# Performance work log

Hardware: AMD Instinct MI355X
Metric: run time of the kernel (lower is better)

Reference implementation:

```python
import jax, jax.numpy as jnp
import numpy as np

N = 50000      # nodes
E = 800000     # edges (before self loops)
F_IN = 64
H = 128
OUT = 1
G = 512        # graphs in batch
NEG_SLOPE = 0.2


def setup_inputs() -> dict:
    key = jax.random.key(0)
    ks = jax.random.split(key, 16)
    s_in = 1.0 / np.sqrt(F_IN)
    s_h = 1.0 / np.sqrt(H)
    return {
        "x": jax.random.normal(ks[0], (N, F_IN), jnp.float32),
        "edge_index": jax.random.randint(ks[1], (2, E), 0, N, jnp.int64),
        "edge_weight": jax.random.uniform(ks[2], (E,), jnp.float32),
        "batch": jnp.sort(jax.random.randint(ks[3], (N,), 0, G, jnp.int64)),
        # GATv2 layer 1 (lin_l, lin_r, att, bias)
        "Wl1": jax.random.normal(ks[4], (F_IN, H), jnp.float32) * s_in,
        "bl1": jnp.zeros((H,), jnp.float32),
        "Wr1": jax.random.normal(ks[5], (F_IN, H), jnp.float32) * s_in,
        "br1": jnp.zeros((H,), jnp.float32),
        "att1": jax.random.normal(ks[6], (H,), jnp.float32) * s_h,
        "b1": jnp.zeros((H,), jnp.float32),
        # GATv2 layer 2
        "Wl2": jax.random.normal(ks[7], (H, H), jnp.float32) * s_h,
        "bl2": jnp.zeros((H,), jnp.float32),
        "Wr2": jax.random.normal(ks[8], (H, H), jnp.float32) * s_h,
        "br2": jnp.zeros((H,), jnp.float32),
        "att2": jax.random.normal(ks[9], (H,), jnp.float32) * s_h,
        "b2": jnp.zeros((H,), jnp.float32),
        # final linear head
        "Wlin": jax.random.normal(ks[10], (H, OUT), jnp.float32) * s_h,
        "blin": jnp.zeros((OUT,), jnp.float32),
    }


def gatv2_conv(x, src, dst, Wl, bl, Wr, br, att, bias):
    """PyG GATv2Conv, heads=1: alpha = softmax_dst(att . leaky_relu(xl[src]+xr[dst]));
    out[dst] = sum alpha * xl[src] + bias. Self loops already in (src, dst)."""
    xl = x @ Wl + bl                       # [N,H]  source transform
    xr = x @ Wr + br                       # [N,H]  destination transform
    e = xl[src] + xr[dst]                  # [Etot,H]
    logits = jax.nn.leaky_relu(e, NEG_SLOPE) @ att   # [Etot]
    # segment softmax over destination nodes (self loops -> every node nonempty)
    m = jax.ops.segment_max(logits, dst, num_segments=N)
    ea = jnp.exp(logits - m[dst])
    denom = jax.ops.segment_sum(ea, dst, num_segments=N)
    alpha = ea / denom[dst]
    out = jax.ops.segment_sum(alpha[:, None] * xl[src], dst, num_segments=N)
    return out + bias


def reference(x, edge_index, edge_weight, batch,
              Wl1, bl1, Wr1, br1, att1, b1,
              Wl2, bl2, Wr2, br2, att2, b2,
              Wlin, blin):
    # add self loops (GATv2Conv default add_self_loops=True); edge_weight unused by GATv2
    loops = jnp.arange(N, dtype=edge_index.dtype)
    src = jnp.concatenate([edge_index[0], loops])
    dst = jnp.concatenate([edge_index[1], loops])

    h = jax.nn.relu(gatv2_conv(x, src, dst, Wl1, bl1, Wr1, br1, att1, b1))
    h = jax.nn.relu(gatv2_conv(h, src, dst, Wl2, bl2, Wr2, br2, att2, b2))

    # global mean pool over graphs
    sums = jax.ops.segment_sum(h, batch, num_segments=G)          # [G,H]
    cnt = jax.ops.segment_sum(jnp.ones((N,), h.dtype), batch, num_segments=G)
    pooled = sums / jnp.maximum(cnt, 1.0)[:, None]

    return pooled @ Wlin + blin                                   # [G,OUT]
```

## Files before the change

### kernel.cpp

```cpp
#include <hip/hip_runtime.h>
#include <hip/hip_fp16.h>
#include <math.h>

#define N_NODES 50000
#define N_EDGES 800000
#define F_IN    64
#define H_DIM   128
#define N_GRAPH 512
#define NEG_SLOPE 0.2f
#define SCAN_NB ((N_NODES + 255) / 256)

typedef __attribute__((ext_vector_type(8))) short short8;
typedef __attribute__((ext_vector_type(4))) float f32x4;
typedef __attribute__((ext_vector_type(2))) float f32x2;

__device__ __forceinline__ void bsplit(float v, unsigned short& h, unsigned short& l) {
    unsigned u = __float_as_uint(v);
    h = (unsigned short)(u >> 16);
    float hf = __uint_as_float(u & 0xFFFF0000u);
    float r = v - hf;
    l = (unsigned short)(__float_as_uint(r) >> 16);
}
__device__ __forceinline__ float bjoin(unsigned short h, unsigned short l) {
    return __uint_as_float(((unsigned)h) << 16) + __uint_as_float(((unsigned)l) << 16);
}

#define NB_PX 3125
#define NB_PW 192
#define NB_H  3125
__global__ __launch_bounds__(256) void k_prep(
    const float* __restrict__ x,
    const float* __restrict__ Wl1, const float* __restrict__ Wr1,
    const float* __restrict__ Wl2, const float* __restrict__ Wr2,
    const int* __restrict__ dst,
    unsigned short* __restrict__ Xhi, unsigned short* __restrict__ Xlo,
    unsigned short* __restrict__ WThi, unsigned short* __restrict__ WTlo,
    int* __restrict__ counts, int* __restrict__ rank)
{
    const int bid = blockIdx.x, tid = threadIdx.x;
    if (bid < NB_PX) {
        int i4 = (bid * 256 + tid) * 4;
        if (i4 < N_NODES * F_IN) {
            float4 v = *(const float4*)(x + i4);
            ushort4 h, l;
            bsplit(v.x, h.x, l.x); bsplit(v.y, h.y, l.y);
            bsplit(v.z, h.z, l.z); bsplit(v.w, h.w, l.w);
            *(ushort4*)(Xhi + i4) = h;
            *(ushort4*)(Xlo + i4) = l;
        }
    } else if (bid < NB_PX + NB_PW) {
        int idx = (bid - NB_PX) * 256 + tid;
        if (idx < 49152) {
            const float* W; int K, li, base, o;
            if (idx < 8192)       { W = Wl1; K = 64;  li = idx;         base = 0;     o = 0; }
            else if (idx < 16384) { W = Wr1; K = 64;  li = idx - 8192;  base = 0;     o = 1; }
            else if (idx < 32768) { W = Wl2; K = 128; li = idx - 16384; base = 16384; o = 0; }
            else                  { W = Wr2; K = 128; li = idx - 32768; base = 16384; o = 1; }
            int c = li / K, k = li - c * K;
            int g = c >> 4, n16 = c & 15;
            int kkblk = k >> 5, quad = (k >> 3) & 3, j = k & 7;
            int off = base + kkblk * 8192 + o * 4096 + g * 512 + (quad * 16 + n16) * 8 + j;
            unsigned short h, l;
            bsplit(W[k * 128 + c], h, l);
            WThi[off] = h; WTlo[off] = l;
        }
    } else {
        int e = (bid - NB_PX - NB_PW) * 256 + tid;
        if (e < N_EDGES) {
            int pos = atomicAdd(&counts[dst[e]], 1);
            rank[e] = pos;
        }
    }
}

__global__ __launch_bounds__(256) void k_scan1(const int* __restrict__ counts,
                                               int* __restrict__ excl,
                                               int* __restrict__ partials) {
    __shared__ int s[256];
    int t = threadIdx.x, gid = blockIdx.x * 256 + t;
    int v = (gid < N_NODES) ? counts[gid] : 0;
    s[t] = v;
    __syncthreads();
    for (int off = 1; off < 256; off <<= 1) {
        int x = (t >= off) ? s[t - off] : 0;
        __syncthreads();
        s[t] += x;
        __syncthreads();
    }
    if (gid < N_NODES) excl[gid] = s[t] - v;
    if (t == 255) partials[blockIdx.x] = s[t];
}

__global__ __launch_bounds__(256) void k_scan3(int* __restrict__ offsets,
                                               const int* __restrict__ partials) {
    __shared__ int s[256];
    const int t = threadIdx.x, b = blockIdx.x;
    int v = (t < SCAN_NB) ? partials[t] : 0;
    s[t] = v;
    __syncthreads();
    for (int off = 1; off < 256; off <<= 1) {
        int x = (t >= off) ? s[t - off] : 0;
        __syncthreads();
        s[t] += x;
        __syncthreads();
    }
    int base = (b > 0) ? s[b - 1] : 0;
    int gid = b * 256 + t;
    if (gid < N_NODES) offsets[gid] += base;
    if (gid == 0) offsets[N_NODES] = N_EDGES;
}

__global__ __launch_bounds__(256) void k_fill(const int* __restrict__ src,
                                              const int* __restrict__ dst,
                                              const int* __restrict__ offsets,
                                              const int* __restrict__ rank,
                                              int* __restrict__ col_src) {
    int e = blockIdx.x * 256 + threadIdx.x;
    if (e < N_EDGES) {
        col_src[offsets[dst[e]] + rank[e]] = src[e];
    }
}

#define APITCH 40
#define GB_GEMM ((N_NODES + 63) / 64)
__global__ __launch_bounds__(256, 4) void k_gemm_mfma(
    const unsigned short* __restrict__ Xhi, const unsigned short* __restrict__ Xlo,
    const unsigned short* __restrict__ WThi, const unsigned short* __restrict__ WTlo,
    const float* __restrict__ bl, const float* __restrict__ br,
    unsigned short* __restrict__ OL, unsigned short* __restrict__ OR_, int K)
{
    __shared__ __align__(16) unsigned short Ah[64 * APITCH];
    __shared__ __align__(16) unsigned short Al[64 * APITCH];

    const int tid  = threadIdx.x;
    const int wv   = tid >> 6;
    const int lane = tid & 63;
    const int n16  = lane & 15;
    const int quad = lane >> 4;
    const int row0 = blockIdx.x * 64;

    f32x4 acc[4][2][2];
#pragma unroll
    for (int r = 0; r < 4; ++r)
#pragma unroll
        for (int c = 0; c < 2; ++c)
#pragma unroll
            for (int o = 0; o < 2; ++o) acc[r][c][o] = (f32x4)0.f;

    for (int kk = 0; kk < K; kk += 32) {
#pragma unroll
        for (int jj = 0; jj < 2; ++jj) {
            int j = tid + jj * 256;
            int part = j >> 8;
            int r = (j & 255) >> 2, sub = j & 3;
            int grow = row0 + r;
            const unsigned short* s = (part ? Xlo : Xhi) + (size_t)grow * K + kk + sub * 8;
            unsigned short* dl = (part ? Al : Ah) + r * APITCH + sub * 8;
            uint4 v = make_uint4(0u, 0u, 0u, 0u);
            if (grow < N_NODES) v = *(const uint4*)s;
            *(uint4*)dl = v;
        }
        __syncthreads();

        const unsigned short* wb_h = WThi + (size_t)(kk >> 5) * 8192;
        const unsigned short* wb_l = WTlo + (size_t)(kk >> 5) * 8192;
        short8 bh[2][2], bo[2][2];
#pragma unroll
        for (int c = 0; c < 2; ++c)
#pragma unroll
            for (int o = 0; o < 2; ++o) {
                size_t off = (size_t)o * 4096 + (size_t)(wv * 2 + c) * 512 + (size_t)lane * 8;
                bh[c][o] = *(const short8*)(wb_h + off);
                bo[c][o] = *(const short8*)(wb_l + off);
            }
#pragma unroll
        for (int r = 0; r < 4; ++r) {
            int rl = r * 16 + n16;
            short8 ah = *(const short8*)(Ah + rl * APITCH + quad * 8);
            short8 al = *(const short8*)(Al + rl * APITCH + quad * 8);
#pragma unroll
            for (int c = 0; c < 2; ++c)
#pragma unroll
                for (int o = 0; o < 2; ++o) {
                    f32x4 t = acc[r][c][o];
                    t = __builtin_amdgcn_mfma_f32_16x16x32_bf16(ah, bh[c][o], t, 0, 0, 0);
                    t = __builtin_amdgcn_mfma_f32_16x16x32_bf16(ah, bo[c][o], t, 0, 0, 0);
                    t = __builtin_amdgcn_mfma_f32_16x16x32_bf16(al, bh[c][o], t, 0, 0, 0);
                    acc[r][c][o] = t;
                }
        }
        __syncthreads();
    }

#pragma unroll
    for (int r = 0; r < 4; ++r)
#pragma unroll
        for (int c = 0; c < 2; ++c)
#pragma unroll
            for (int o = 0; o < 2; ++o) {
                int col = wv * 32 + c * 16 + n16;
                float bb = (o ? br : bl)[col];
                unsigned short* O = o ? OR_ : OL;
#pragma unroll
                for (int g = 0; g < 4; ++g) {
                    int grow = row0 + r * 16 + quad * 4 + g;
                    if (grow < N_NODES) {
                        __half hv = __float2half(acc[r][c][o][g] + bb);
                        O[(size_t)grow * 128 + col] = *(unsigned short*)&hv;
                    }
                }
            }
}

__device__ __forceinline__ float red16dpp(float v) {
    v += __int_as_float(__builtin_amdgcn_update_dpp(
             0, __float_as_int(v), 0xB1, 0xF, 0xF, true));
    v += __int_as_float(__builtin_amdgcn_update_dpp(
             0, __float_as_int(v), 0x4E, 0xF, 0xF, true));
    v += __int_as_float(__builtin_amdgcn_update_dpp(
             0, __float_as_int(v), 0x141, 0xF, 0xF, true));
    v += __int_as_float(__builtin_amdgcn_update_dpp(
             0, __float_as_int(v), 0x140, 0xF, 0xF, true));
    return v;
}

__device__ __forceinline__ void load_h8v(const unsigned short* base, size_t off,
                                         f32x2 x[4]) {
    uint4 u = *(const uint4*)(base + off);
    float2 a = __half22float2(*(__half2*)&u.x);
    float2 b = __half22float2(*(__half2*)&u.y);
    float2 c = __half22float2(*(__half2*)&u.z);
    float2 d = __half22float2(*(__half2*)&u.w);
    f32x2 v0 = {a.x, a.y}; x[0] = v0;
    f32x2 v1 = {b.x, b.y}; x[1] = v1;
    f32x2 v2 = {c.x, c.y}; x[2] = v2;
    f32x2 v3 = {d.x, d.y}; x[3] = v3;
}

__device__ __forceinline__ float dot8lk(const f32x2 x[4], const f32x2 r[4],
                                        const f32x2 a[4]) {
    f32x2 e0 = x[0] + r[0];
    f32x2 e1 = x[1] + r[1];
    f32x2 l0 = __builtin_elementwise_max(e0, NEG_SLOPE * e0);
    f32x2 l1 = __builtin_elementwise_max(e1, NEG_SLOPE * e1);
    f32x2 s0 = a[0] * l0;
    f32x2 s1 = a[1] * l1;
    f32x2 e2 = x[2] + r[2];
    f32x2 e3 = x[3] + r[3];
    f32x2 l2 = __builtin_elementwise_max(e2, NEG_SLOPE * e2);
    f32x2 l3 = __builtin_elementwise_max(e3, NEG_SLOPE * e3);
    s0 += a[2] * l2;
    s1 += a[3] * l3;
    f32x2 s = s0 + s1;
    return s.x + s.y;
}

__global__ __launch_bounds__(256) void k_edge(
    const unsigned short* __restrict__ xl, const unsigned short* __restrict__ xr,
    const float* __restrict__ att, const float* __restrict__ bias,
    const int* __restrict__ offsets, const int* __restrict__ col_src,
    unsigned short* __restrict__ outHi, unsigned short* __restrict__ outLo)
{
    int d = blockIdx.x * 4 + (threadIdx.x >> 6);
    if (d >= N_NODES) return;
    const int lane = threadIdx.x & 63;
    const int q = lane >> 4;
    const int t = lane & 15;
    const size_t dim0 = (size_t)t * 8;

    f32x2 rr[4], aa[4], xs[4];
    load_h8v(xr, (size_t)d * 128 + dim0, rr);
    {
        const float4 a0 = *(const float4*)(att + dim0);
        const float4 a1 = *(const float4*)(att + dim0 + 4);
        f32x2 w0 = {a0.x, a0.y}; aa[0] = w0;
        f32x2 w1 = {a0.z, a0.w}; aa[1] = w1;
        f32x2 w2 = {a1.x, a1.y}; aa[2] = w2;
        f32x2 w3 = {a1.z, a1.w}; aa[3] = w3;
    }
    load_h8v(xl, (size_t)d * 128 + dim0, xs);
    float sl = red16dpp(dot8lk(xs, rr, aa));

    float m = sl, thr = sl + 8.f;
    float lsum = (q == 0) ? 1.f : 0.f;
    f32x2 zero = {0.f, 0.f};
    f32x2 acc[4];
#pragma unroll
    for (int j = 0; j < 4; ++j) acc[j] = (q == 0) ? xs[j] : zero;

    const int ibeg = offsets[d], iend = offsets[d + 1];
    for (int base = ibeg; base < iend; base += 4) {
        int i = base + q;
        bool valid = (i < iend);
        int s = valid ? col_src[i] : d;
        f32x2 x[4];
        load_h8v(xl, (size_t)s * 128 + dim0, x);
        float logit = red16dpp(dot8lk(x, rr, aa));
        if (__builtin_expect(logit > thr, 0)) {
            float sc = __expf(m - logit);
            lsum *= sc;
#pragma unroll
            for (int j = 0; j < 4; ++j) acc[j] = acc[j] * sc;
            m = logit; thr = logit + 8.f;
        }
        float w = valid ? __expf(logit - m) : 0.f;
        lsum += w;
        f32x2 w2 = {w, w};
#pragma unroll
        for (int j = 0; j < 4; ++j) acc[j] += w2 * x[j];
    }

    float M = m;
    M = fmaxf(M, __shfl_xor(M, 16));
    M = fmaxf(M, __shfl_xor(M, 32));
    float sc = __expf(m - M);
    lsum *= sc;
    f32x2 sc2 = {sc, sc};
#pragma unroll
    for (int j = 0; j < 4; ++j) acc[j] = acc[j] * sc2;
#pragma unroll
    for (int off = 16; off <= 32; off <<= 1) {
        lsum += __shfl_xor(lsum, off);
#pragma unroll
        for (int j = 0; j < 4; ++j) {
            acc[j].x += __shfl_xor(acc[j].x, off);
            acc[j].y += __shfl_xor(acc[j].y, off);
        }
    }

    if (q == 0) {
        float inv = 1.f / lsum;
        const float4 b0 = *(const float4*)(bias + dim0);
        const float4 b1 = *(const float4*)(bias + dim0 + 4);
        float bv[8] = {b0.x, b0.y, b0.z, b0.w, b1.x, b1.y, b1.z, b1.w};
        float v[8];
#pragma unroll
        for (int j = 0; j < 4; ++j) {
            v[2 * j]     = fmaxf(fmaf(acc[j].x, inv, bv[2 * j]), 0.f);
            v[2 * j + 1] = fmaxf(fmaf(acc[j].y, inv, bv[2 * j + 1]), 0.f);
        }
        union { unsigned short s[8]; uint4 u; } Hh, Ll;
#pragma unroll
        for (int i2 = 0; i2 < 8; ++i2) bsplit(v[i2], Hh.s[i2], Ll.s[i2]);
        *(uint4*)(outHi + (size_t)d * 128 + dim0) = Hh.u;
        *(uint4*)(outLo + (size_t)d * 128 + dim0) = Ll.u;
    }
}

__global__ __launch_bounds__(256) void k_pool(
    const unsigned short* __restrict__ hHi, const unsigned short* __restrict__ hLo,
    const int* __restrict__ batch,
    float* __restrict__ psum, float* __restrict__ pcnt)
{
    const int tid = threadIdx.x;
    const int tx = tid & 31;
    const int ty = tid >> 5;
    const int n0 = blockIdx.x * 64;
    const int d0 = tx * 4;

    float4 acc = make_float4(0.f, 0.f, 0.f, 0.f);
    int cur = -1, crun = 0;
#pragma unroll
    for (int it = 0; it < 8; ++it) {
        int n = n0 + it * 8 + ty;
        if (n < N_NODES) {
            int g = batch[n];
            if (g != cur) {
                if (cur >= 0) {
                    atomicAdd(&psum[cur * 128 + d0 + 0], acc.x);
                    atomicAdd(&psum[cur * 128 + d0 + 1], acc.y);
                    atomicAdd(&psum[cur * 128 + d0 + 2], acc.z);
                    atomicAdd(&psum[cur * 128 + d0 + 3], acc.w);
                    if (tx == 0) atomicAdd(&pcnt[cur], (float)crun);
                }
                cur = g; acc = make_float4(0.f, 0.f, 0.f, 0.f); crun = 0;
            }
            ushort4 h = *(const ushort4*)(hHi + (size_t)n * 128 + d0);
            ushort4 l = *(const ushort4*)(hLo + (size_t)n * 128 + d0);
            acc.x += bjoin(h.x, l.x);
            acc.y += bjoin(h.y, l.y);
            acc.z += bjoin(h.z, l.z);
            acc.w += bjoin(h.w, l.w);
            crun++;
        }
    }
    if (cur >= 0) {
        atomicAdd(&psum[cur * 128 + d0 + 0], acc.x);
        atomicAdd(&psum[cur * 128 + d0 + 1], acc.y);
        atomicAdd(&psum[cur * 128 + d0 + 2], acc.z);
        atomicAdd(&psum[cur * 128 + d0 + 3], acc.w);
        if (tx == 0) atomicAdd(&pcnt[cur], (float)crun);
    }
}

__global__ __launch_bounds__(256) void k_head(
    const float* __restrict__ psum, const float* __restrict__ pcnt,
    const float* __restrict__ Wlin, const float* __restrict__ blin,
    float* __restrict__ out)
{
    int g = blockIdx.x * 4 + (threadIdx.x >> 6);
    if (g >= N_GRAPH) return;
    int lane = threadIdx.x & 63;
    float c = fmaxf(pcnt[g], 1.f);
    float2 s = *(const float2*)(psum + (size_t)g * 128 + lane * 2);
    float p = (s.x * Wlin[lane * 2] + s.y * Wlin[lane * 2 + 1]) / c;
#pragma unroll
    for (int off = 32; off > 0; off >>= 1) p += __shfl_xor(p, off);
    if (lane == 0) out[g] = p + blin[0];
}

extern "C" void kernel_launch(void* const* d_in, const int* in_sizes, int n_in,
                              void* d_out, int out_size, void* d_ws, size_t ws_size,
                              hipStream_t stream) {
    const float* x     = (const float*)d_in[0];
    const int*   ei    = (const int*)d_in[1];
    const int*   batch = (const int*)d_in[3];
    const float* Wl1 = (const float*)d_in[4],  *bl1 = (const float*)d_in[5];
    const float* Wr1 = (const float*)d_in[6],  *br1 = (const float*)d_in[7];
    const float* att1= (const float*)d_in[8],  *b1  = (const float*)d_in[9];
    const float* Wl2 = (const float*)d_in[10], *bl2 = (const float*)d_in[11];
    const float* Wr2 = (const float*)d_in[12], *br2 = (const float*)d_in[13];
    const float* att2= (const float*)d_in[14], *b2  = (const float*)d_in[15];
    const float* Wlin= (const float*)d_in[16], *blin= (const float*)d_in[17];
    float* out = (float*)d_out;

    const int* src = ei;
    const int* dst = ei + N_EDGES;

    char* p = (char*)d_ws;
    auto carve = [&](size_t bytes) {
        void* r = (void*)p;
        p += (bytes + 255) & ~(size_t)255;
        return r;
    };
    unsigned short* bufA   = (unsigned short*)carve((size_t)N_NODES * 128 * 2);
    unsigned short* bufB   = (unsigned short*)carve((size_t)N_NODES * 128 * 2);
    unsigned short* Hhi    = (unsigned short*)carve((size_t)N_NODES * 128 * 2);
    unsigned short* Hlo    = (unsigned short*)carve((size_t)N_NODES * 128 * 2);
    unsigned short* Xhi1   = (unsigned short*)carve((size_t)N_NODES * 64 * 2);
    unsigned short* Xlo1   = (unsigned short*)carve((size_t)N_NODES * 64 * 2);
    unsigned short* WThi   = (unsigned short*)carve(49152 * 2);
    unsigned short* WTlo   = (unsigned short*)carve(49152 * 2);
    int*            offsets= (int*)carve((size_t)(N_NODES + 1) * 4);
    int*            rank   = (int*)carve((size_t)N_EDGES * 4);
    int*            partials=(int*)carve(256 * 4);
    int*            col_src= (int*)carve((size_t)N_EDGES * 4);
    char* zb = (char*)carve(200192 + 262144 + 2048);
    int*   counts = (int*)zb;
    float* psum   = (float*)(zb + 200192);
    float* pcnt   = (float*)(zb + 200192 + 262144);
    const size_t zbytes = 200192 + 262144 + 2048;

    hipMemsetAsync(zb, 0, zbytes, stream);

    k_prep<<<NB_PX + NB_PW + NB_H, 256, 0, stream>>>(
        x, Wl1, Wr1, Wl2, Wr2, dst,
        Xhi1, Xlo1, WThi, WTlo, counts, rank);
    k_scan1<<<SCAN_NB, 256, 0, stream>>>(counts, offsets, partials);
    k_scan3<<<SCAN_NB, 256, 0, stream>>>(offsets, partials);
    k_fill <<<(N_EDGES + 255) / 256, 256, 0, stream>>>(src, dst, offsets, rank, col_src);

    k_gemm_mfma<<<GB_GEMM, 256, 0, stream>>>(Xhi1, Xlo1, WThi, WTlo,
                                             bl1, br1, bufA, bufB, F_IN);
    k_edge<<<(N_NODES + 3) / 4, 256, 0, stream>>>(
        bufA, bufB, att1, b1, offsets, col_src, Hhi, Hlo);
    k_gemm_mfma<<<GB_GEMM, 256, 0, stream>>>(Hhi, Hlo, WThi + 16384, WTlo + 16384,
                                             bl2, br2, bufA, bufB, H_DIM);
    k_edge<<<(N_NODES + 3) / 4, 256, 0, stream>>>(
        bufA, bufB, att2, b2, offsets, col_src, Hhi, Hlo);
    k_pool<<<(N_NODES + 63) / 64, 256, 0, stream>>>(Hhi, Hlo, batch, psum, pcnt);
    k_head<<<(N_GRAPH + 3) / 4, 256, 0, stream>>>(psum, pcnt, Wlin, blin, out);
}
```

Before: 304.3 us.

## Fuse dst histogram into first GEMM launch and pad counters to cache lines

Moves the per-edge atomic histogram out of the prep kernel and into extra blocks of the first-layer GEMM launch, so the atomic-heavy edge counting can run alongside the MFMA GEMM blocks. The per-node counters are also spaced 16 ints apart (one 64-byte slot each) to reduce atomic contention and false sharing on shared cache lines. The cost is a larger memset (3.2MB instead of 200KB) and strided reads in the scan.

```diff
diff --git a/kernel.cpp b/kernel.cpp
--- a/kernel.cpp
+++ b/kernel.cpp
@@ -27,15 +27,12 @@
 
 #define NB_PX 3125
 #define NB_PW 192
-#define NB_H  3125
 __global__ __launch_bounds__(256) void k_prep(
     const float* __restrict__ x,
     const float* __restrict__ Wl1, const float* __restrict__ Wr1,
     const float* __restrict__ Wl2, const float* __restrict__ Wr2,
-    const int* __restrict__ dst,
     unsigned short* __restrict__ Xhi, unsigned short* __restrict__ Xlo,
-    unsigned short* __restrict__ WThi, unsigned short* __restrict__ WTlo,
-    int* __restrict__ counts, int* __restrict__ rank)
+    unsigned short* __restrict__ WThi, unsigned short* __restrict__ WTlo)
 {
     const int bid = blockIdx.x, tid = threadIdx.x;
     if (bid < NB_PX) {
@@ -48,7 +45,7 @@
             *(ushort4*)(Xhi + i4) = h;
             *(ushort4*)(Xlo + i4) = l;
         }
-    } else if (bid < NB_PX + NB_PW) {
+    } else {
         int idx = (bid - NB_PX) * 256 + tid;
         if (idx < 49152) {
             const float* W; int K, li, base, o;
@@ -64,12 +61,6 @@
             bsplit(W[k * 128 + c], h, l);
             WThi[off] = h; WTlo[off] = l;
         }
-    } else {
-        int e = (bid - NB_PX - NB_PW) * 256 + tid;
-        if (e < N_EDGES) {
-            int pos = atomicAdd(&counts[dst[e]], 1);
-            rank[e] = pos;
-        }
     }
 }
 
@@ -78,7 +69,7 @@
                                                int* __restrict__ partials) {
     __shared__ int s[256];
     int t = threadIdx.x, gid = blockIdx.x * 256 + t;
-    int v = (gid < N_NODES) ? counts[gid] : 0;
+    int v = (gid < N_NODES) ? counts[gid << 4] : 0;
     s[t] = v;
     __syncthreads();
     for (int off = 1; off < 256; off <<= 1) {
@@ -123,21 +114,22 @@
 
 #define APITCH 40
 #define GB_GEMM ((N_NODES + 63) / 64)
-__global__ __launch_bounds__(256, 4) void k_gemm_mfma(
+#define GB_HIST ((N_EDGES + 255) / 256)
+
+__device__ __forceinline__ void gemm_body(
+    unsigned short* __restrict__ Ah, unsigned short* __restrict__ Al,
     const unsigned short* __restrict__ Xhi, const unsigned short* __restrict__ Xlo,
     const unsigned short* __restrict__ WThi, const unsigned short* __restrict__ WTlo,
     const float* __restrict__ bl, const float* __restrict__ br,
-    unsigned short* __restrict__ OL, unsigned short* __restrict__ OR_, int K)
-{
-    __shared__ __align__(16) unsigned short Ah[64 * APITCH];
-    __shared__ __align__(16) unsigned short Al[64 * APITCH];
-
+    unsigned short* __restrict__ OL, unsigned short* __restrict__ OR_,
+    int K, int blk)
+{
     const int tid  = threadIdx.x;
     const int wv   = tid >> 6;
     const int lane = tid & 63;
     const int n16  = lane & 15;
     const int quad = lane >> 4;
-    const int row0 = blockIdx.x * 64;
+    const int row0 = blk * 64;
 
     f32x4 acc[4][2][2];
 #pragma unroll
@@ -210,6 +202,36 @@
                     }
                 }
             }
+}
+
+__global__ __launch_bounds__(256, 4) void k_gemm_mfma(
+    const unsigned short* __restrict__ Xhi, const unsigned short* __restrict__ Xlo,
+    const unsigned short* __restrict__ WThi, const unsigned short* __restrict__ WTlo,
+    const float* __restrict__ bl, const float* __restrict__ br,
+    unsigned short* __restrict__ OL, unsigned short* __restrict__ OR_, int K)
+{
+    __shared__ __align__(16) unsigned short Ah[64 * APITCH];
+    __shared__ __align__(16) unsigned short Al[64 * APITCH];
+    gemm_body(Ah, Al, Xhi, Xlo, WThi, WTlo, bl, br, OL, OR_, K, blockIdx.x);
+}
+
+__global__ __launch_bounds__(256, 4) void k_gemm1_hist(
+    const unsigned short* __restrict__ Xhi, const unsigned short* __restrict__ Xlo,
+    const unsigned short* __restrict__ WThi, const unsigned short* __restrict__ WTlo,
+    const float* __restrict__ bl, const float* __restrict__ br,
+    unsigned short* __restrict__ OL, unsigned short* __restrict__ OR_, int K,
+    const int* __restrict__ dst, int* __restrict__ counts, int* __restrict__ rank)
+{
+    __shared__ __align__(16) unsigned short Ah[64 * APITCH];
+    __shared__ __align__(16) unsigned short Al[64 * APITCH];
+    if (blockIdx.x < GB_GEMM) {
+        gemm_body(Ah, Al, Xhi, Xlo, WThi, WTlo, bl, br, OL, OR_, K, blockIdx.x);
+    } else {
+        int e = (blockIdx.x - GB_GEMM) * 256 + threadIdx.x;
+        if (e < N_EDGES) {
+            rank[e] = atomicAdd(&counts[dst[e] << 4], 1);
+        }
+    }
 }
 
 __device__ __forceinline__ float red16dpp(float v) {
@@ -445,23 +467,26 @@
     int*            rank   = (int*)carve((size_t)N_EDGES * 4);
     int*            partials=(int*)carve(256 * 4);
     int*            col_src= (int*)carve((size_t)N_EDGES * 4);
-    char* zb = (char*)carve(200192 + 262144 + 2048);
+    const size_t counts_bytes = (size_t)N_NODES * 64;
+    char* zb = (char*)carve(counts_bytes + 262144 + 2048);
     int*   counts = (int*)zb;
-    float* psum   = (float*)(zb + 200192);
-    float* pcnt   = (float*)(zb + 200192 + 262144);
-    const size_t zbytes = 200192 + 262144 + 2048;
+    float* psum   = (float*)(zb + counts_bytes);
+    float* pcnt   = (float*)(zb + counts_bytes + 262144);
+    const size_t zbytes = counts_bytes + 262144 + 2048;
 
     hipMemsetAsync(zb, 0, zbytes, stream);
 
-    k_prep<<<NB_PX + NB_PW + NB_H, 256, 0, stream>>>(
-        x, Wl1, Wr1, Wl2, Wr2, dst,
-        Xhi1, Xlo1, WThi, WTlo, counts, rank);
+    k_prep<<<NB_PX + NB_PW, 256, 0, stream>>>(
+        x, Wl1, Wr1, Wl2, Wr2, Xhi1, Xlo1, WThi, WTlo);
+
+    k_gemm1_hist<<<GB_GEMM + GB_HIST, 256, 0, stream>>>(
+        Xhi1, Xlo1, WThi, WTlo, bl1, br1, bufA, bufB, F_IN,
+        dst, counts, rank);
+
     k_scan1<<<SCAN_NB, 256, 0, stream>>>(counts, offsets, partials);
     k_scan3<<<SCAN_NB, 256, 0, stream>>>(offsets, partials);
     k_fill <<<(N_EDGES + 255) / 256, 256, 0, stream>>>(src, dst, offsets, rank, col_src);
 
-    k_gemm_mfma<<<GB_GEMM, 256, 0, stream>>>(Xhi1, Xlo1, WThi, WTlo,
-                                             bl1, br1, bufA, bufB, F_IN);
     k_edge<<<(N_NODES + 3) / 4, 256, 0, stream>>>(
         bufA, bufB, att1, b1, offsets, col_src, Hhi, Hlo);
     k_gemm_mfma<<<GB_GEMM, 256, 0, stream>>>(Hhi, Hlo, WThi + 16384, WTlo + 16384,
```

Result: no change. 299.5 us (-1.6%).

## Build CSR with two-level LDS bin sort instead of global atomic counting

Applied to the files above, without the earlier changes.

Replaces the per-destination global atomicAdd counting sort with a two-level bucket sort. Edges are first binned into 256-node buckets using shared-memory atomics per 2048-edge block. A block-major scan then gives bucket offsets, and a per-bucket kernel sorts edges locally by destination and writes CSR offsets and source indices. Source and local destination are packed into one 32-bit word, which relies on node ids fitting in 16 bits. The first GEMM is also launched before the CSR build so it no longer waits on it. The final stage runs only 196 blocks, which may underuse the GPU, and it adds more kernel launches.

```diff
diff --git a/kernel.cpp b/kernel.cpp
--- a/kernel.cpp
+++ b/kernel.cpp
@@ -8,11 +8,15 @@
 #define H_DIM   128
 #define N_GRAPH 512
 #define NEG_SLOPE 0.2f
-#define SCAN_NB ((N_NODES + 255) / 256)
 
 typedef __attribute__((ext_vector_type(8))) short short8;
 typedef __attribute__((ext_vector_type(4))) float f32x4;
 typedef __attribute__((ext_vector_type(2))) float f32x2;
+
+#define NBIN   196
+#define NBLK1  391
+#define NBB    (NBIN * NBLK1)
+#define SCANA_NB ((NBB + 255) / 256)
 
 __device__ __forceinline__ void bsplit(float v, unsigned short& h, unsigned short& l) {
     unsigned u = __float_as_uint(v);
@@ -27,7 +31,6 @@
 
 #define NB_PX 3125
 #define NB_PW 192
-#define NB_H  3125
 __global__ __launch_bounds__(256) void k_prep(
     const float* __restrict__ x,
     const float* __restrict__ Wl1, const float* __restrict__ Wr1,
@@ -35,8 +38,9 @@
     const int* __restrict__ dst,
     unsigned short* __restrict__ Xhi, unsigned short* __restrict__ Xlo,
     unsigned short* __restrict__ WThi, unsigned short* __restrict__ WTlo,
-    int* __restrict__ counts, int* __restrict__ rank)
+    int* __restrict__ lrank, int* __restrict__ bcnt)
 {
+    __shared__ int cnt_lds[NBIN];
     const int bid = blockIdx.x, tid = threadIdx.x;
     if (bid < NB_PX) {
         int i4 = (bid * 256 + tid) * 4;
@@ -65,20 +69,28 @@
             WThi[off] = h; WTlo[off] = l;
         }
     } else {
-        int e = (bid - NB_PX - NB_PW) * 256 + tid;
-        if (e < N_EDGES) {
-            int pos = atomicAdd(&counts[dst[e]], 1);
-            rank[e] = pos;
-        }
-    }
-}
-
-__global__ __launch_bounds__(256) void k_scan1(const int* __restrict__ counts,
-                                               int* __restrict__ excl,
+        const int b2 = bid - NB_PX - NB_PW;
+        if (tid < NBIN) cnt_lds[tid] = 0;
+        __syncthreads();
+#pragma unroll
+        for (int it = 0; it < 8; ++it) {
+            int e = b2 * 2048 + it * 256 + tid;
+            if (e < N_EDGES) {
+                int d = dst[e];
+                lrank[e] = atomicAdd(&cnt_lds[d >> 8], 1);
+            }
+        }
+        __syncthreads();
+        if (tid < NBIN) bcnt[tid * NBLK1 + b2] = cnt_lds[tid];
+    }
+}
+
+__global__ __launch_bounds__(256) void k_scanA(const int* __restrict__ bcnt,
+                                               int* __restrict__ bbase,
                                                int* __restrict__ partials) {
     __shared__ int s[256];
     int t = threadIdx.x, gid = blockIdx.x * 256 + t;
-    int v = (gid < N_NODES) ? counts[gid] : 0;
+    int v = (gid < NBB) ? bcnt[gid] : 0;
     s[t] = v;
     __syncthreads();
     for (int off = 1; off < 256; off <<= 1) {
@@ -87,37 +99,77 @@
         s[t] += x;
         __syncthreads();
     }
-    if (gid < N_NODES) excl[gid] = s[t] - v;
+    if (gid < NBB) bbase[gid] = s[t] - v;
     if (t == 255) partials[blockIdx.x] = s[t];
 }
 
-__global__ __launch_bounds__(256) void k_scan3(int* __restrict__ offsets,
+__global__ __launch_bounds__(256) void k_scanB(int* __restrict__ bbase,
                                                const int* __restrict__ partials) {
-    __shared__ int s[256];
+    __shared__ int red[256];
     const int t = threadIdx.x, b = blockIdx.x;
-    int v = (t < SCAN_NB) ? partials[t] : 0;
-    s[t] = v;
+    int acc = 0;
+    for (int j = t; j < b; j += 256) acc += partials[j];
+    red[t] = acc;
+    __syncthreads();
+    for (int off = 128; off > 0; off >>= 1) {
+        if (t < off) red[t] += red[t + off];
+        __syncthreads();
+    }
+    int base = red[0];
+    int gid = b * 256 + t;
+    if (gid < NBB) bbase[gid] += base;
+}
+
+__global__ __launch_bounds__(256) void k_bin2(const int* __restrict__ src,
+                                              const int* __restrict__ dst,
+                                              const int* __restrict__ lrank,
+                                              const int* __restrict__ bbase,
+                                              unsigned* __restrict__ ebin) {
+    int e = blockIdx.x * 256 + threadIdx.x;
+    if (e < N_EDGES) {
+        int d = dst[e];
+        int pos = bbase[(d >> 8) * NBLK1 + (e >> 11)] + lrank[e];
+        ebin[pos] = (unsigned)src[e] | ((unsigned)(d & 255) << 16);
+    }
+}
+
+__global__ __launch_bounds__(256) void k_bin3(const unsigned* __restrict__ ebin,
+                                              const int* __restrict__ bbase,
+                                              int* __restrict__ offsets,
+                                              int* __restrict__ col_src) {
+    __shared__ int cnt2[256];
+    __shared__ int sc[256];
+    __shared__ int cur[256];
+    const int b = blockIdx.x, t = threadIdx.x;
+    const int lo = bbase[b * NBLK1];
+    const int hi = (b == NBIN - 1) ? N_EDGES : bbase[(b + 1) * NBLK1];
+
+    cnt2[t] = 0;
+    __syncthreads();
+    for (int pos = lo + t; pos < hi; pos += 256) {
+        unsigned u = ebin[pos];
+        atomicAdd(&cnt2[u >> 16], 1);
+    }
+    __syncthreads();
+    int v = cnt2[t];
+    sc[t] = v;
     __syncthreads();
     for (int off = 1; off < 256; off <<= 1) {
-        int x = (t >= off) ? s[t - off] : 0;
-        __syncthreads();
-        s[t] += x;
-        __syncthreads();
-    }
-    int base = (b > 0) ? s[b - 1] : 0;
-    int gid = b * 256 + t;
-    if (gid < N_NODES) offsets[gid] += base;
-    if (gid == 0) offsets[N_NODES] = N_EDGES;
-}
-
-__global__ __launch_bounds__(256) void k_fill(const int* __restrict__ src,
-                                              const int* __restrict__ dst,
-                                              const int* __restrict__ offsets,
-                                              const int* __restrict__ rank,
-                                              int* __restrict__ col_src) {
-    int e = blockIdx.x * 256 + threadIdx.x;
-    if (e < N_EDGES) {
-        col_src[offsets[dst[e]] + rank[e]] = src[e];
+        int x = (t >= off) ? sc[t - off] : 0;
+        __syncthreads();
+        sc[t] += x;
+        __syncthreads();
+    }
+    int myoff = lo + sc[t] - v;
+    int node = b * 256 + t;
+    if (node < N_NODES) offsets[node] = myoff;
+    cur[t] = myoff;
+    if (b == NBIN - 1 && t == 0) offsets[N_NODES] = N_EDGES;
+    __syncthreads();
+    for (int pos = lo + t; pos < hi; pos += 256) {
+        unsigned u = ebin[pos];
+        int p = atomicAdd(&cur[u >> 16], 1);
+        col_src[p] = (int)(u & 0xFFFFu);
     }
 }
 
@@ -442,26 +494,31 @@
     unsigned short* WThi   = (unsigned short*)carve(49152 * 2);
     unsigned short* WTlo   = (unsigned short*)carve(49152 * 2);
     int*            offsets= (int*)carve((size_t)(N_NODES + 1) * 4);
-    int*            rank   = (int*)carve((size_t)N_EDGES * 4);
-    int*            partials=(int*)carve(256 * 4);
+    int*            lrank  = (int*)carve((size_t)N_EDGES * 4);
+    int*            bcnt   = (int*)carve((size_t)NBB * 4);
+    int*            bbase  = (int*)carve((size_t)NBB * 4);
+    int*            partials=(int*)carve(SCANA_NB * 4);
+    unsigned*       ebin   = (unsigned*)carve((size_t)N_EDGES * 4);
     int*            col_src= (int*)carve((size_t)N_EDGES * 4);
-    char* zb = (char*)carve(200192 + 262144 + 2048);
-    int*   counts = (int*)zb;
-    float* psum   = (float*)(zb + 200192);
-    float* pcnt   = (float*)(zb + 200192 + 262144);
-    const size_t zbytes = 200192 + 262144 + 2048;
+    char* zb = (char*)carve(262144 + 2048);
+    float* psum   = (float*)zb;
+    float* pcnt   = (float*)(zb + 262144);
+    const size_t zbytes = 262144 + 2048;
 
     hipMemsetAsync(zb, 0, zbytes, stream);
 
-    k_prep<<<NB_PX + NB_PW + NB_H, 256, 0, stream>>>(
+    k_prep<<<NB_PX + NB_PW + NBLK1, 256, 0, stream>>>(
         x, Wl1, Wr1, Wl2, Wr2, dst,
-        Xhi1, Xlo1, WThi, WTlo, counts, rank);
-    k_scan1<<<SCAN_NB, 256, 0, stream>>>(counts, offsets, partials);
-    k_scan3<<<SCAN_NB, 256, 0, stream>>>(offsets, partials);
-    k_fill <<<(N_EDGES + 255) / 256, 256, 0, stream>>>(src, dst, offsets, rank, col_src);
+        Xhi1, Xlo1, WThi, WTlo, lrank, bcnt);
 
     k_gemm_mfma<<<GB_GEMM, 256, 0, stream>>>(Xhi1, Xlo1, WThi, WTlo,
                                              bl1, br1, bufA, bufB, F_IN);
+
+    k_scanA<<<SCANA_NB, 256, 0, stream>>>(bcnt, bbase, partials);
+    k_scanB<<<SCANA_NB, 256, 0, stream>>>(bbase, partials);
+    k_bin2 <<<(N_EDGES + 255) / 256, 256, 0, stream>>>(src, dst, lrank, bbase, ebin);
+    k_bin3 <<<NBIN, 256, 0, stream>>>(ebin, bbase, offsets, col_src);
+
     k_edge<<<(N_NODES + 3) / 4, 256, 0, stream>>>(
         bufA, bufB, att1, b1, offsets, col_src, Hhi, Hlo);
     k_gemm_mfma<<<GB_GEMM, 256, 0, stream>>>(Hhi, Hlo, WThi + 16384, WTlo + 16384,
```

New measurement: 286.6 us. 1.06x faster.
